# Optimization experiments

Hardware: AMD Instinct MI355X
Metric: run time of the kernel (lower is better)

Reference implementation:

```python
import jax, jax.numpy as jnp
import numpy as np

B, N, DIM, HEADS = 8, 4096, 512, 8
BASE = 10000.0


def rope_cos_sin(n, dim, base=BASE):
    k_max = dim // 2
    theta = 1.0 / base ** (jnp.arange(k_max, dtype=jnp.float32) / k_max)
    angles = jnp.arange(n, dtype=jnp.float32)[:, None] * theta  # (n, k_max)
    return jnp.cos(angles), jnp.sin(angles)


def apply_rope(x, cos, sin):
    # x: (b, n, dim); complex pairs are interleaved (even=real, odd=imag)
    xr = x[..., 0::2]
    xi = x[..., 1::2]
    out_r = cos * xr - sin * xi
    out_i = sin * xr + cos * xi
    return jnp.stack([out_r, out_i], axis=-1).reshape(x.shape)


def setup_inputs() -> dict:
    key = jax.random.key(0)
    ks = jax.random.split(key, 8)
    s = 0.02
    return {
        'x': jax.random.normal(ks[0], (B, N, DIM), jnp.float32),
        'y': jax.random.normal(ks[1], (B, N, DIM), jnp.float32),
        'Wq': jax.random.normal(ks[2], (DIM, DIM), jnp.float32) * s,
        'bq': jax.random.normal(ks[3], (DIM,), jnp.float32) * s,
        'Wk': jax.random.normal(ks[4], (DIM, DIM), jnp.float32) * s,
        'bk': jax.random.normal(ks[5], (DIM,), jnp.float32) * s,
        'lepe_w': jax.random.normal(ks[6], (DIM, 1, 3), jnp.float32) * s,
        'lepe_b': jax.random.normal(ks[7], (DIM,), jnp.float32) * s,
    }


def reference(x, y, Wq, bq, Wk, bk, lepe_w, lepe_b):
    b, n, c = x.shape
    h = HEADS
    d = c // h
    q = jax.nn.elu(x @ Wq.T + bq) + 1.0
    k = jax.nn.elu(y @ Wk.T + bk) + 1.0
    cos, sin = rope_cos_sin(n, c)
    q_rope = apply_rope(q, cos, sin).reshape(b, n, h, d).transpose(0, 2, 1, 3)
    k_rope = apply_rope(k, cos, sin).reshape(b, n, h, d).transpose(0, 2, 1, 3)
    qh = q.reshape(b, n, h, d).transpose(0, 2, 1, 3)
    kh = k.reshape(b, n, h, d).transpose(0, 2, 1, 3)
    v = y.reshape(b, n, h, d).transpose(0, 2, 1, 3)
    kmean = kh.mean(axis=2, keepdims=True)  # (b,h,1,d)
    z = 1.0 / (jnp.einsum('bhnd,bhmd->bhnm', qh, kmean) + 1e-6)  # (b,h,n,1)
    scale = n ** (-0.5)
    kv = jnp.einsum('bhnd,bhne->bhde', k_rope * scale, v * scale)  # (b,h,d,d)
    out = jnp.einsum('bhnd,bhde->bhne', q_rope, kv) * z  # (b,h,n,d)
    out = out.transpose(0, 2, 1, 3).reshape(b, n, c)
    # LePE: depthwise conv1d over value stream
    vc = v.transpose(0, 2, 1, 3).reshape(b, n, c).transpose(0, 2, 1)  # (b,c,n)
    lepe = jax.lax.conv_general_dilated(
        vc, lepe_w, window_strides=(1,), padding=[(1, 1)],
        dimension_numbers=('NCH', 'OIH', 'NCH'), feature_group_count=c)
    lepe = lepe + lepe_b[None, :, None]
    return out + lepe.transpose(0, 2, 1)
```

## Files before the change

kernel.cpp:

```cpp
#include <hip/hip_runtime.h>

#define B_ 8
#define N_ 4096
#define C_ 512
#define H_ 8

typedef _Float16 h8  __attribute__((ext_vector_type(8)));
typedef _Float16 h4v __attribute__((ext_vector_type(4)));
typedef float    f4  __attribute__((ext_vector_type(4)));

static const size_t OFF_CT   = 0;
static const size_t OFF_XH   = (size_t)8*1024*1024;
static const size_t OFF_YH   = (size_t)40*1024*1024;
static const size_t OFF_WQH  = (size_t)72*1024*1024;
static const size_t OFF_WKH  = (size_t)72*1024*1024 + 512*1024;
static const size_t OFF_KSUM = (size_t)73*1024*1024;
static const size_t OFF_KVG  = (size_t)73*1024*1024 + 64*1024;
static const size_t OFF_KVT  = (size_t)74*1024*1024 + 64*1024;

__device__ __forceinline__ unsigned int pack2h(float a, float b){
    union { _Float16 h[2]; unsigned int u; } x;
    x.h[0] = (_Float16)a; x.h[1] = (_Float16)b; return x.u;
}
__device__ __forceinline__ void unpack2h(unsigned int u, float& a, float& b){
    union { unsigned int u; _Float16 h[2]; } x; x.u = u;
    a = (float)x.h[0]; b = (float)x.h[1];
}

__global__ __launch_bounds__(256) void k_prep(
    const float* __restrict__ y,
    const float* __restrict__ Wq, const float* __restrict__ Wk,
    _Float16* __restrict__ yh,
    _Float16* __restrict__ Wqh, _Float16* __restrict__ Wkh,
    unsigned int* __restrict__ ct)
{
    int bid = blockIdx.x;
    if (bid >= 8448){
        int jj = bid - 8448, t = threadIdx.x;
        double th = exp((double)jj * -0.035977892078031970);
        float thf = (float)th;
#pragma unroll
        for (int i=0;i<16;++i){
            int n = i*256 + t;
            float s, c; sincosf((float)n * thf, &s, &c);
            ct[(size_t)jj*4096 + n] = pack2h(c, s);
        }
        return;
    }
    const float* src; _Float16* dst; size_t base;
    if (bid < 8192)       { src = y;  dst = yh;  base = (size_t)bid*2048; }
    else if (bid < 8320)  { src = Wq; dst = Wqh; base = (size_t)(bid-8192)*2048; }
    else                  { src = Wk; dst = Wkh; base = (size_t)(bid-8320)*2048; }
    size_t o = base + (size_t)threadIdx.x*8;
    float4 a = *(const float4*)&src[o];
    float4 b = *(const float4*)&src[o+4];
    uint4 r; r.x = pack2h(a.x,a.y); r.y = pack2h(a.z,a.w); r.z = pack2h(b.x,b.y); r.w = pack2h(b.z,b.w);
    *(uint4*)&dst[o] = r;
}

__device__ __forceinline__ void stage_a64(const _Float16* __restrict__ g, _Float16* lds, int t){
    int r = t >> 2;
    int j = (t & 3) ^ ((r ^ (r >> 2)) & 3);
    __builtin_amdgcn_global_load_lds(
        (const __attribute__((address_space(1))) void*)(g + (size_t)r*C_ + j*8),
        (__attribute__((address_space(3))) void*)(lds + (size_t)(t & 192)*8),
        16, 0, 0);
}
__device__ __forceinline__ void stage_b128(const _Float16* __restrict__ g, _Float16* lds, int t){
#pragma unroll
    for (int i=0;i<2;++i){
        int u = i*256 + t;
        int r = u >> 2;
        int j = (u & 3) ^ ((r ^ (r >> 2)) & 3);
        __builtin_amdgcn_global_load_lds(
            (const __attribute__((address_space(1))) void*)(g + (size_t)r*C_ + j*8),
            (__attribute__((address_space(3))) void*)(lds + (size_t)(i*256 + (t & 192))*8),
            16, 0, 0);
    }
}

template<int IS_Q>
__global__ __launch_bounds__(256, 4) void k_gemm(
    const _Float16* __restrict__ A, const _Float16* __restrict__ Wh, const float* __restrict__ bias,
    const unsigned int* __restrict__ ct,
    float* __restrict__ ksum, const float* __restrict__ ksumIn,
    float* __restrict__ kvg, const _Float16* __restrict__ kvTg,
    const _Float16* __restrict__ yh, const float* __restrict__ lw, const float* __restrict__ lb,
    float* __restrict__ outp,
    const float* __restrict__ x32, _Float16* __restrict__ xh16)
{
    __shared__ __align__(16) char smem[36864];
    _Float16* qrs = (_Float16*)smem;
    unsigned int* krsU = (unsigned int*)smem;
    unsigned int* vsU  = (unsigned int*)(smem + 16384);

    if constexpr (!IS_Q){
        if (blockIdx.y >= 512){
            int cb = (blockIdx.y - 512)*4 + blockIdx.x;
#pragma unroll 4
            for (int it=0; it<32; ++it){
                size_t o = ((size_t)(cb*32 + it))*2048 + (size_t)threadIdx.x*8;
                float4 a = *(const float4*)&x32[o];
                float4 b = *(const float4*)&x32[o+4];
                uint4 r; r.x = pack2h(a.x,a.y); r.y = pack2h(a.z,a.w);
                r.z = pack2h(b.x,b.y); r.w = pack2h(b.z,b.w);
                *(uint4*)&xh16[o] = r;
            }
            return;
        }
    }

    const int t = threadIdx.x;
    const int lane = t & 63;
    const int w = t >> 6;
    const int wm = w >> 1, wn = w & 1;
    const int d_lin = blockIdx.x + (blockIdx.y << 2);
    const int xcd = d_lin & 7;
    const int sq  = d_lin >> 3;
    const int col0 = (sq & 3) * 128;
    const int row0 = (xcd * 64 + (sq >> 2)) * 64;
    const int lrow = lane & 15, lg = lane >> 4;
    const int b = row0 >> 12;

    f4 acc[2][4] = {};
    const _Float16* Ab = A  + (size_t)row0*C_;
    const _Float16* Bb = Wh + (size_t)col0*C_;
    stage_a64 (Ab,      (_Float16*)(smem),               t);
    stage_b128(Bb,      (_Float16*)(smem + 12288),       t);
    stage_a64 (Ab + 32, (_Float16*)(smem + 4096),        t);
    stage_b128(Bb + 32, (_Float16*)(smem + 12288 + 8192),t);

    const int sw = (lrow ^ (lrow >> 2)) & 3;
    const int cK = (lg ^ sw) * 8;

#pragma unroll
    for (int kk=0; kk<16; ++kk){
        if (kk < 15) asm volatile("s_waitcnt vmcnt(3)" ::: "memory");
        else         asm volatile("s_waitcnt vmcnt(0)" ::: "memory");
        __builtin_amdgcn_s_barrier();
        if (kk < 14){
            const int ss = (kk+2)%3;
            stage_a64 (Ab + (kk+2)*32, (_Float16*)(smem + ss*4096),         t);
            stage_b128(Bb + (kk+2)*32, (_Float16*)(smem + 12288 + ss*8192), t);
        }
        const int sc = kk%3;
        const _Float16* As = (const _Float16*)(smem + sc*4096);
        const _Float16* Bs = (const _Float16*)(smem + 12288 + sc*8192);
        h8 af[2], bf[4];
#pragma unroll
        for (int mi=0; mi<2; ++mi) af[mi] = *(const h8*)&As[(wm*32 + mi*16 + lrow)*32 + cK];
#pragma unroll
        for (int ni=0; ni<4; ++ni) bf[ni] = *(const h8*)&Bs[(wn*64 + ni*16 + lrow)*32 + cK];
#pragma unroll
        for (int mi=0; mi<2; ++mi)
#pragma unroll
            for (int ni=0; ni<4; ++ni)
                acc[mi][ni] = __builtin_amdgcn_mfma_f32_16x16x32_f16(af[mi], bf[ni], acc[mi][ni], 0,0,0);
    }
    __syncthreads();

    const int hcol0 = col0 + wn*64;
    float bcol[4], km[4];
#pragma unroll
    for (int ni=0; ni<4; ++ni){
        int c = hcol0 + ni*16 + lrow;
        bcol[ni] = bias[c];
        km[ni] = IS_Q ? ksumIn[b*C_ + c] * (1.0f/4096.0f) : 0.0f;
    }
    float colsum[4] = {0.f,0.f,0.f,0.f};
    float zr[2][4];
    _Float16* qw = qrs + w*2304;

#pragma unroll
    for (int mi=0; mi<2; ++mi){
        float qv[4][4];
#pragma unroll
        for (int ni=0; ni<4; ++ni)
#pragma unroll
            for (int r=0; r<4; ++r){
                float v = acc[mi][ni][r] + bcol[ni];
                qv[ni][r] = v > 0.f ? v + 1.f : __expf(v);
            }
        if constexpr (IS_Q){
#pragma unroll
            for (int r=0; r<4; ++r){
                float p = qv[0][r]*km[0] + qv[1][r]*km[1] + qv[2][r]*km[2] + qv[3][r]*km[3];
                p += __shfl_xor(p, 1); p += __shfl_xor(p, 2);
                p += __shfl_xor(p, 4); p += __shfl_xor(p, 8);
                zr[mi][r] = 1.0f / (p + 1e-6f);
            }
        } else {
#pragma unroll
            for (int ni=0; ni<4; ++ni)
                colsum[ni] += qv[ni][0]+qv[ni][1]+qv[ni][2]+qv[ni][3];
        }
        const int n0 = (row0 & (N_-1)) + wm*32 + mi*16 + lg*4;
#pragma unroll
        for (int ni=0; ni<4; ++ni){
            int c = hcol0 + ni*16 + lrow;
            int jj = c >> 1;
            uint4 tu = *(const uint4*)&ct[(size_t)jj*4096 + n0];
            float cs4[4], sn4[4];
            unpack2h(tu.x, cs4[0], sn4[0]);
            unpack2h(tu.y, cs4[1], sn4[1]);
            unpack2h(tu.z, cs4[2], sn4[2]);
            unpack2h(tu.w, cs4[3], sn4[3]);
            float rv[4];
#pragma unroll
            for (int r=0; r<4; ++r){
                float val = qv[ni][r];
                float par = __shfl_xor(val, 1);
                rv[r] = (lane & 1) ? fmaf(sn4[r], par, cs4[r]*val) : fmaf(cs4[r], val, -sn4[r]*par);
            }
            if constexpr (IS_Q){
#pragma unroll
                for (int r=0; r<4; ++r){
                    float prv = __shfl_xor(rv[r], 1);
                    if (!(lane & 1))
                        *(unsigned int*)&qw[(mi*16 + lg*4 + r)*72 + (ni*16 + lrow)] = pack2h(rv[r], prv);
                }
            } else {
                int d = ni*16 + lrow;
                int n2 = wm*16 + mi*8 + lg*2;
                unsigned int* p = &krsU[wn*2048 + d*32 + (n2 ^ ((d & 7) << 2))];
                uint2 pr; pr.x = pack2h(rv[0], rv[1]); pr.y = pack2h(rv[2], rv[3]);
                *(uint2*)p = pr;
            }
        }
    }

    if constexpr (!IS_Q){
#pragma unroll
        for (int ni=0; ni<4; ++ni){
            float s = colsum[ni];
            s += __shfl_xor(s, 16); s += __shfl_xor(s, 32);
            if (lane < 16) atomicAdd(&ksum[b*C_ + hcol0 + ni*16 + lane], s);
        }
        {
            const int grp = lane >> 4, li = lane & 15;
#pragma unroll
            for (int it=0; it<8; ++it){
                int g = it*4 + w;
                int hl = g >> 4, q = g & 15;
                int row = q*4 + grp;
                uint2 mine = *(const uint2*)&yh[(size_t)(row0 + row)*C_ + col0 + hl*64 + li*4];
                uint2 oth; oth.x = __shfl_xor(mine.x, 16); oth.y = __shfl_xor(mine.y, 16);
                if (!(grp & 1)){
                    int n2 = row >> 1;
#pragma unroll
                    for (int e=0; e<4; ++e){
                        int ea = li*4 + e;
                        unsigned int mf = ((e<2 ? mine.x : mine.y) >> ((e&1)*16)) & 0xffffu;
                        unsigned int of = ((e<2 ? oth.x  : oth.y ) >> ((e&1)*16)) & 0xffffu;
                        vsU[hl*2048 + ea*32 + (n2 ^ ((ea & 7) << 2))] = mf | (of << 16);
                    }
                }
            }
        }
        __syncthreads();
        f4 acc2[2][4] = {};
        const unsigned int* krsW = krsU + wn*2048;
        const unsigned int* vsW  = vsU  + wn*2048;
#pragma unroll
        for (int ks=0; ks<2; ++ks){
            h8 a2[2], b2[4];
#pragma unroll
            for (int mi2=0; mi2<2; ++mi2){
                int d = wm*32 + mi2*16 + lrow;
                int c4 = (ks*16 + lg*4) ^ ((d & 7) << 2);
                a2[mi2] = *(const h8*)&krsW[d*32 + c4];
            }
#pragma unroll
            for (int ni2=0; ni2<4; ++ni2){
                int e = ni2*16 + lrow;
                int c4 = (ks*16 + lg*4) ^ ((e & 7) << 2);
                b2[ni2] = *(const h8*)&vsW[e*32 + c4];
            }
#pragma unroll
            for (int mi2=0; mi2<2; ++mi2)
#pragma unroll
                for (int ni2=0; ni2<4; ++ni2)
                    acc2[mi2][ni2] = __builtin_amdgcn_mfma_f32_16x16x32_f16(a2[mi2], b2[ni2], acc2[mi2][ni2], 0,0,0);
        }
        const int bh = b*H_ + (col0 >> 6) + wn;
#pragma unroll
        for (int mi2=0; mi2<2; ++mi2)
#pragma unroll
            for (int ni2=0; ni2<4; ++ni2)
#pragma unroll
                for (int rr=0; rr<4; ++rr){
                    int d = wm*32 + mi2*16 + lg*4 + rr;
                    int e = ni2*16 + lrow;
                    atomicAdd(&kvg[(size_t)bh*4096 + d*64 + e], acc2[mi2][ni2][rr] * (1.0f/4096.0f));
                }
    } else {
        const int bhh = b*H_ + (col0 >> 6) + wn;
        h8 kv0[4], kv1[4];
#pragma unroll
        for (int ni2=0; ni2<4; ++ni2){
            int e = ni2*16 + lrow;
            kv0[ni2] = *(const h8*)&kvTg[(size_t)bhh*4096 + e*64 + lg*8];
            kv1[ni2] = *(const h8*)&kvTg[(size_t)bhh*4096 + e*64 + 32 + lg*8];
        }
        __syncthreads();
        f4 acc2[2][4] = {};
#pragma unroll
        for (int mi2=0; mi2<2; ++mi2){
            h8 a0 = *(const h8*)&qw[(mi2*16 + lrow)*72 + 0*32 + lg*8];
            h8 a1 = *(const h8*)&qw[(mi2*16 + lrow)*72 + 1*32 + lg*8];
#pragma unroll
            for (int ni2=0; ni2<4; ++ni2){
                acc2[mi2][ni2] = __builtin_amdgcn_mfma_f32_16x16x32_f16(a0, kv0[ni2], acc2[mi2][ni2], 0,0,0);
                acc2[mi2][ni2] = __builtin_amdgcn_mfma_f32_16x16x32_f16(a1, kv1[ni2], acc2[mi2][ni2], 0,0,0);
            }
        }
#pragma unroll
        for (int mi2=0; mi2<2; ++mi2){
#pragma unroll
            for (int r=0; r<4; ++r){
                float z = zr[mi2][r];
#pragma unroll
                for (int ni2=0; ni2<4; ++ni2){
                    float val = acc2[mi2][ni2][r] * z;
                    float pv = __shfl_xor(val, 1);
                    if (!(lane & 1))
                        *(unsigned int*)&qw[(mi2*16 + lg*4 + r)*72 + (ni2*16 + lrow)] = pack2h(val, pv);
                }
            }
        }
        __syncthreads();
        const int cg = t & 31;
        const int c4p = cg * 4;
        const int hl = c4p >> 6;
        const int e0 = c4p & 63;
        float w0[4], w1[4], w2[4], wb[4];
#pragma unroll
        for (int j=0;j<4;++j){
            int cc = col0 + c4p + j;
            w0[j]=lw[cc*3+0]; w1[j]=lw[cc*3+1]; w2[j]=lw[cc*3+2]; wb[j]=lb[cc];
        }
#pragma unroll
        for (int i=0;i<8;++i){
            int rl = (t >> 5) + i*8;
            int grow = row0 + rl;
            int nloc = grow & (N_-1);
            int wreg = ((rl >> 5) << 1) + hl;
            h4v a = *(const h4v*)&qrs[wreg*2304 + (rl & 31)*72 + e0];
            const _Float16* yp = yh + (size_t)grow*C_ + col0 + c4p;
            h4v y1 = *(const h4v*)yp;
            float s0 = fmaf((float)y1[0], w1[0], wb[0]);
            float s1 = fmaf((float)y1[1], w1[1], wb[1]);
            float s2 = fmaf((float)y1[2], w1[2], wb[2]);
            float s3 = fmaf((float)y1[3], w1[3], wb[3]);
            if (nloc > 0){
                h4v y0 = *(const h4v*)(yp - C_);
                s0 = fmaf((float)y0[0], w0[0], s0); s1 = fmaf((float)y0[1], w0[1], s1);
                s2 = fmaf((float)y0[2], w0[2], s2); s3 = fmaf((float)y0[3], w0[3], s3);
            }
            if (nloc < N_-1){
                h4v y2 = *(const h4v*)(yp + C_);
                s0 = fmaf((float)y2[0], w2[0], s0); s1 = fmaf((float)y2[1], w2[1], s1);
                s2 = fmaf((float)y2[2], w2[2], s2); s3 = fmaf((float)y2[3], w2[3], s3);
            }
            float4 o;
            o.x = (float)a[0] + s0; o.y = (float)a[1] + s1;
            o.z = (float)a[2] + s2; o.w = (float)a[3] + s3;
            *(float4*)&outp[(size_t)grow*C_ + col0 + c4p] = o;
        }
    }
}

__global__ __launch_bounds__(256) void k_kvmerge(const float* __restrict__ kvg, _Float16* __restrict__ kvTg){
    int bh = blockIdx.x, t = threadIdx.x;
    const float* src = kvg + (size_t)bh*4096;
    _Float16* dst = kvTg + (size_t)bh*4096;
#pragma unroll
    for (int i=0;i<4;++i){
        int q = i*256 + t;
        int e2 = q & 31, d2 = q >> 5;
        float2 a0 = *(const float2*)&src[(2*d2)*64 + 2*e2];
        float2 a1 = *(const float2*)&src[(2*d2+1)*64 + 2*e2];
        *(unsigned int*)&dst[(2*e2)*64 + 2*d2]   = pack2h(a0.x, a1.x);
        *(unsigned int*)&dst[(2*e2+1)*64 + 2*d2] = pack2h(a0.y, a1.y);
    }
}

extern "C" void kernel_launch(void* const* d_in, const int* in_sizes, int n_in,
                              void* d_out, int out_size, void* d_ws, size_t ws_size,
                              hipStream_t stream)
{
    (void)in_sizes; (void)n_in; (void)out_size; (void)ws_size;
    const float* x  = (const float*)d_in[0];
    const float* y  = (const float*)d_in[1];
    const float* Wq = (const float*)d_in[2];
    const float* bq = (const float*)d_in[3];
    const float* Wk = (const float*)d_in[4];
    const float* bk = (const float*)d_in[5];
    const float* lw = (const float*)d_in[6];
    const float* lb = (const float*)d_in[7];

    char* ws = (char*)d_ws;
    unsigned int* ct = (unsigned int*)(ws + OFF_CT);
    _Float16* xh   = (_Float16*)(ws + OFF_XH);
    _Float16* yh   = (_Float16*)(ws + OFF_YH);
    _Float16* Wqh  = (_Float16*)(ws + OFF_WQH);
    _Float16* Wkh  = (_Float16*)(ws + OFF_WKH);
    float*    ksum = (float*)(ws + OFF_KSUM);
    float*    kvg  = (float*)(ws + OFF_KVG);
    _Float16* kvTg = (_Float16*)(ws + OFF_KVT);
    float*    out  = (float*)d_out;

    hipMemsetAsync(ws + OFF_KSUM, 0, 64*1024 + 1024*1024, stream);
    k_prep<<<dim3(8704), dim3(256), 0, stream>>>(y, Wq, Wk, yh, Wqh, Wkh, ct);
    k_gemm<0><<<dim3(4, 576), dim3(256), 0, stream>>>(yh, Wkh, bk, ct,
        ksum, nullptr, kvg, nullptr, yh, nullptr, nullptr, nullptr, x, xh);
    k_kvmerge<<<dim3(64), dim3(256), 0, stream>>>(kvg, kvTg);
    k_gemm<1><<<dim3(4, 512), dim3(256), 0, stream>>>(xh, Wqh, bq, ct,
        nullptr, ksum, nullptr, kvTg, yh, lw, lb, out, nullptr, nullptr);
}
```

Measured before the change: 185.2 us.

## Switch projection GEMMs to single-wave blocks reading operands directly from global

Both GEMM kernels now launch one 64-thread wavefront per block, with 64x64 tiles for K and 32x64 tiles for Q. Each block covers exactly one head's columns. The LDS-staged triple-buffered global_load_lds pipeline and its barriers are removed, so MFMA fragments load straight from global memory into registers. The aim is to cut barrier and LDS traffic and raise occupancy through more, smaller blocks. The cost is redundant global and L2 reads of the A and W operands with no shared-memory reuse across waves.

```diff
diff --git a/kernel.cpp b/kernel.cpp
--- a/kernel.cpp
+++ b/kernel.cpp
@@ -58,29 +58,8 @@
     *(uint4*)&dst[o] = r;
 }
 
-__device__ __forceinline__ void stage_a64(const _Float16* __restrict__ g, _Float16* lds, int t){
-    int r = t >> 2;
-    int j = (t & 3) ^ ((r ^ (r >> 2)) & 3);
-    __builtin_amdgcn_global_load_lds(
-        (const __attribute__((address_space(1))) void*)(g + (size_t)r*C_ + j*8),
-        (__attribute__((address_space(3))) void*)(lds + (size_t)(t & 192)*8),
-        16, 0, 0);
-}
-__device__ __forceinline__ void stage_b128(const _Float16* __restrict__ g, _Float16* lds, int t){
-#pragma unroll
-    for (int i=0;i<2;++i){
-        int u = i*256 + t;
-        int r = u >> 2;
-        int j = (u & 3) ^ ((r ^ (r >> 2)) & 3);
-        __builtin_amdgcn_global_load_lds(
-            (const __attribute__((address_space(1))) void*)(g + (size_t)r*C_ + j*8),
-            (__attribute__((address_space(3))) void*)(lds + (size_t)(i*256 + (t & 192))*8),
-            16, 0, 0);
-    }
-}
-
-template<int IS_Q>
-__global__ __launch_bounds__(256, 4) void k_gemm(
+template<int IS_Q, int MI>
+__global__ __launch_bounds__(64, IS_Q ? 4 : 3) void k_gemm(
     const _Float16* __restrict__ A, const _Float16* __restrict__ Wh, const float* __restrict__ bias,
     const unsigned int* __restrict__ ct,
     float* __restrict__ ksum, const float* __restrict__ ksumIn,
@@ -89,17 +68,18 @@
     float* __restrict__ outp,
     const float* __restrict__ x32, _Float16* __restrict__ xh16)
 {
-    __shared__ __align__(16) char smem[36864];
-    _Float16* qrs = (_Float16*)smem;
-    unsigned int* krsU = (unsigned int*)smem;
-    unsigned int* vsU  = (unsigned int*)(smem + 16384);
+    __shared__ __align__(16) char smem[IS_Q ? 4608 : 16384];
+    _Float16* qw = (_Float16*)smem;
+    unsigned int* krU = (unsigned int*)smem;
+    unsigned int* vU  = (unsigned int*)(smem + 8192);
 
     if constexpr (!IS_Q){
         if (blockIdx.y >= 512){
-            int cb = (blockIdx.y - 512)*4 + blockIdx.x;
+            int cb = (blockIdx.y - 512)*8 + blockIdx.x;
+            int t = threadIdx.x;
 #pragma unroll 4
-            for (int it=0; it<32; ++it){
-                size_t o = ((size_t)(cb*32 + it))*2048 + (size_t)threadIdx.x*8;
+            for (int it=0; it<128; ++it){
+                size_t o = ((size_t)cb*128 + it)*512 + (size_t)t*8;
                 float4 a = *(const float4*)&x32[o];
                 float4 b = *(const float4*)&x32[o+4];
                 uint4 r; r.x = pack2h(a.x,a.y); r.y = pack2h(a.z,a.w);
@@ -111,68 +91,43 @@
     }
 
     const int t = threadIdx.x;
-    const int lane = t & 63;
-    const int w = t >> 6;
-    const int wm = w >> 1, wn = w & 1;
-    const int d_lin = blockIdx.x + (blockIdx.y << 2);
-    const int xcd = d_lin & 7;
-    const int sq  = d_lin >> 3;
-    const int col0 = (sq & 3) * 128;
-    const int row0 = (xcd * 64 + (sq >> 2)) * 64;
-    const int lrow = lane & 15, lg = lane >> 4;
+    const int lrow = t & 15, lg = t >> 4;
+    const int d_lin = blockIdx.x + (blockIdx.y << 3);
+    const int xcd = d_lin & 7, s = d_lin >> 3;
+    const int col0 = (s & 7) * 64;
+    const int row0 = IS_Q ? (xcd*128 + (s >> 3))*32 : (xcd*64 + (s >> 3))*64;
     const int b = row0 >> 12;
-
-    f4 acc[2][4] = {};
-    const _Float16* Ab = A  + (size_t)row0*C_;
-    const _Float16* Bb = Wh + (size_t)col0*C_;
-    stage_a64 (Ab,      (_Float16*)(smem),               t);
-    stage_b128(Bb,      (_Float16*)(smem + 12288),       t);
-    stage_a64 (Ab + 32, (_Float16*)(smem + 4096),        t);
-    stage_b128(Bb + 32, (_Float16*)(smem + 12288 + 8192),t);
-
-    const int sw = (lrow ^ (lrow >> 2)) & 3;
-    const int cK = (lg ^ sw) * 8;
-
+    const int bh = b*H_ + (col0 >> 6);
+
+    f4 acc[MI][4] = {};
+    const _Float16* pa = A  + ((size_t)(row0 + lrow))*C_ + lg*8;
+    const _Float16* pb = Wh + ((size_t)(col0 + lrow))*C_ + lg*8;
 #pragma unroll
     for (int kk=0; kk<16; ++kk){
-        if (kk < 15) asm volatile("s_waitcnt vmcnt(3)" ::: "memory");
-        else         asm volatile("s_waitcnt vmcnt(0)" ::: "memory");
-        __builtin_amdgcn_s_barrier();
-        if (kk < 14){
-            const int ss = (kk+2)%3;
-            stage_a64 (Ab + (kk+2)*32, (_Float16*)(smem + ss*4096),         t);
-            stage_b128(Bb + (kk+2)*32, (_Float16*)(smem + 12288 + ss*8192), t);
-        }
-        const int sc = kk%3;
-        const _Float16* As = (const _Float16*)(smem + sc*4096);
-        const _Float16* Bs = (const _Float16*)(smem + 12288 + sc*8192);
-        h8 af[2], bf[4];
-#pragma unroll
-        for (int mi=0; mi<2; ++mi) af[mi] = *(const h8*)&As[(wm*32 + mi*16 + lrow)*32 + cK];
-#pragma unroll
-        for (int ni=0; ni<4; ++ni) bf[ni] = *(const h8*)&Bs[(wn*64 + ni*16 + lrow)*32 + cK];
-#pragma unroll
-        for (int mi=0; mi<2; ++mi)
+        h8 af[MI], bf[4];
+#pragma unroll
+        for (int mi=0; mi<MI; ++mi) af[mi] = *(const h8*)(pa + (size_t)mi*16*C_ + kk*32);
+#pragma unroll
+        for (int ni=0; ni<4; ++ni)  bf[ni] = *(const h8*)(pb + (size_t)ni*16*C_ + kk*32);
+#pragma unroll
+        for (int mi=0; mi<MI; ++mi)
 #pragma unroll
             for (int ni=0; ni<4; ++ni)
                 acc[mi][ni] = __builtin_amdgcn_mfma_f32_16x16x32_f16(af[mi], bf[ni], acc[mi][ni], 0,0,0);
     }
-    __syncthreads();
-
-    const int hcol0 = col0 + wn*64;
+
     float bcol[4], km[4];
 #pragma unroll
     for (int ni=0; ni<4; ++ni){
-        int c = hcol0 + ni*16 + lrow;
+        int c = col0 + ni*16 + lrow;
         bcol[ni] = bias[c];
         km[ni] = IS_Q ? ksumIn[b*C_ + c] * (1.0f/4096.0f) : 0.0f;
     }
     float colsum[4] = {0.f,0.f,0.f,0.f};
-    float zr[2][4];
-    _Float16* qw = qrs + w*2304;
-
-#pragma unroll
-    for (int mi=0; mi<2; ++mi){
+    float zr[MI][4];
+
+#pragma unroll
+    for (int mi=0; mi<MI; ++mi){
         float qv[4][4];
 #pragma unroll
         for (int ni=0; ni<4; ++ni)
@@ -194,10 +149,10 @@
             for (int ni=0; ni<4; ++ni)
                 colsum[ni] += qv[ni][0]+qv[ni][1]+qv[ni][2]+qv[ni][3];
         }
-        const int n0 = (row0 & (N_-1)) + wm*32 + mi*16 + lg*4;
+        const int n0 = (row0 & (N_-1)) + mi*16 + lg*4;
 #pragma unroll
         for (int ni=0; ni<4; ++ni){
-            int c = hcol0 + ni*16 + lrow;
+            int c = col0 + ni*16 + lrow;
             int jj = c >> 1;
             uint4 tu = *(const uint4*)&ct[(size_t)jj*4096 + n0];
             float cs4[4], sn4[4];
@@ -210,19 +165,19 @@
             for (int r=0; r<4; ++r){
                 float val = qv[ni][r];
                 float par = __shfl_xor(val, 1);
-                rv[r] = (lane & 1) ? fmaf(sn4[r], par, cs4[r]*val) : fmaf(cs4[r], val, -sn4[r]*par);
+                rv[r] = (t & 1) ? fmaf(sn4[r], par, cs4[r]*val) : fmaf(cs4[r], val, -sn4[r]*par);
             }
             if constexpr (IS_Q){
 #pragma unroll
                 for (int r=0; r<4; ++r){
                     float prv = __shfl_xor(rv[r], 1);
-                    if (!(lane & 1))
+                    if (!(t & 1))
                         *(unsigned int*)&qw[(mi*16 + lg*4 + r)*72 + (ni*16 + lrow)] = pack2h(rv[r], prv);
                 }
             } else {
-                int d = ni*16 + lrow;
-                int n2 = wm*16 + mi*8 + lg*2;
-                unsigned int* p = &krsU[wn*2048 + d*32 + (n2 ^ ((d & 7) << 2))];
+                int dd = ni*16 + lrow;
+                int n2 = mi*8 + lg*2;
+                unsigned int* p = &krU[dd*32 + (n2 ^ ((dd & 7) << 2))];
                 uint2 pr; pr.x = pack2h(rv[0], rv[1]); pr.y = pack2h(rv[2], rv[3]);
                 *(uint2*)p = pr;
             }
@@ -232,75 +187,65 @@
     if constexpr (!IS_Q){
 #pragma unroll
         for (int ni=0; ni<4; ++ni){
-            float s = colsum[ni];
-            s += __shfl_xor(s, 16); s += __shfl_xor(s, 32);
-            if (lane < 16) atomicAdd(&ksum[b*C_ + hcol0 + ni*16 + lane], s);
-        }
-        {
-            const int grp = lane >> 4, li = lane & 15;
-#pragma unroll
-            for (int it=0; it<8; ++it){
-                int g = it*4 + w;
-                int hl = g >> 4, q = g & 15;
-                int row = q*4 + grp;
-                uint2 mine = *(const uint2*)&yh[(size_t)(row0 + row)*C_ + col0 + hl*64 + li*4];
-                uint2 oth; oth.x = __shfl_xor(mine.x, 16); oth.y = __shfl_xor(mine.y, 16);
-                if (!(grp & 1)){
-                    int n2 = row >> 1;
-#pragma unroll
-                    for (int e=0; e<4; ++e){
-                        int ea = li*4 + e;
-                        unsigned int mf = ((e<2 ? mine.x : mine.y) >> ((e&1)*16)) & 0xffffu;
-                        unsigned int of = ((e<2 ? oth.x  : oth.y ) >> ((e&1)*16)) & 0xffffu;
-                        vsU[hl*2048 + ea*32 + (n2 ^ ((ea & 7) << 2))] = mf | (of << 16);
-                    }
-                }
-            }
+            float ss = colsum[ni];
+            ss += __shfl_xor(ss, 16); ss += __shfl_xor(ss, 32);
+            if (t < 16) atomicAdd(&ksum[b*C_ + col0 + ni*16 + t], ss);
+        }
+#pragma unroll
+        for (int it=0; it<8; ++it){
+            int n2g = it*4 + lg;
+            int e4 = lrow*4;
+            uint2 r0 = *(const uint2*)&yh[(size_t)(row0 + 2*n2g)*C_ + col0 + e4];
+            uint2 r1 = *(const uint2*)&yh[(size_t)(row0 + 2*n2g + 1)*C_ + col0 + e4];
+            unsigned int v0 = (r0.x & 0xffffu) | (r1.x << 16);
+            unsigned int v1 = (r0.x >> 16)     | (r1.x & 0xffff0000u);
+            unsigned int v2 = (r0.y & 0xffffu) | (r1.y << 16);
+            unsigned int v3 = (r0.y >> 16)     | (r1.y & 0xffff0000u);
+            vU[(e4+0)*32 + (n2g ^ (((e4+0) & 7) << 2))] = v0;
+            vU[(e4+1)*32 + (n2g ^ (((e4+1) & 7) << 2))] = v1;
+            vU[(e4+2)*32 + (n2g ^ (((e4+2) & 7) << 2))] = v2;
+            vU[(e4+3)*32 + (n2g ^ (((e4+3) & 7) << 2))] = v3;
         }
         __syncthreads();
-        f4 acc2[2][4] = {};
-        const unsigned int* krsW = krsU + wn*2048;
-        const unsigned int* vsW  = vsU  + wn*2048;
+        f4 acc2[4][4] = {};
 #pragma unroll
         for (int ks=0; ks<2; ++ks){
-            h8 a2[2], b2[4];
-#pragma unroll
-            for (int mi2=0; mi2<2; ++mi2){
-                int d = wm*32 + mi2*16 + lrow;
-                int c4 = (ks*16 + lg*4) ^ ((d & 7) << 2);
-                a2[mi2] = *(const h8*)&krsW[d*32 + c4];
+            h8 a2[4], b2[4];
+#pragma unroll
+            for (int mi2=0; mi2<4; ++mi2){
+                int dd = mi2*16 + lrow;
+                int c4 = (ks*16 + lg*4) ^ ((dd & 7) << 2);
+                a2[mi2] = *(const h8*)&krU[dd*32 + c4];
             }
 #pragma unroll
             for (int ni2=0; ni2<4; ++ni2){
                 int e = ni2*16 + lrow;
                 int c4 = (ks*16 + lg*4) ^ ((e & 7) << 2);
-                b2[ni2] = *(const h8*)&vsW[e*32 + c4];
-            }
-#pragma unroll
-            for (int mi2=0; mi2<2; ++mi2)
+                b2[ni2] = *(const h8*)&vU[e*32 + c4];
+            }
+#pragma unroll
+            for (int mi2=0; mi2<4; ++mi2)
 #pragma unroll
                 for (int ni2=0; ni2<4; ++ni2)
                     acc2[mi2][ni2] = __builtin_amdgcn_mfma_f32_16x16x32_f16(a2[mi2], b2[ni2], acc2[mi2][ni2], 0,0,0);
         }
-        const int bh = b*H_ + (col0 >> 6) + wn;
-#pragma unroll
-        for (int mi2=0; mi2<2; ++mi2)
+#pragma unroll
+        for (int mi2=0; mi2<4; ++mi2)
 #pragma unroll
             for (int ni2=0; ni2<4; ++ni2)
 #pragma unroll
                 for (int rr=0; rr<4; ++rr){
-                    int d = wm*32 + mi2*16 + lg*4 + rr;
+                    int dd = mi2*16 + lg*4 + rr;
                     int e = ni2*16 + lrow;
-                    atomicAdd(&kvg[(size_t)bh*4096 + d*64 + e], acc2[mi2][ni2][rr] * (1.0f/4096.0f));
+                    atomicAdd(&kvg[(size_t)bh*4096 + dd*64 + e], acc2[mi2][ni2][rr] * (1.0f/4096.0f));
                 }
     } else {
-        const int bhh = b*H_ + (col0 >> 6) + wn;
         h8 kv0[4], kv1[4];
 #pragma unroll
         for (int ni2=0; ni2<4; ++ni2){
             int e = ni2*16 + lrow;
-            kv0[ni2] = *(const h8*)&kvTg[(size_t)bhh*4096 + e*64 + lg*8];
-            kv1[ni2] = *(const h8*)&kvTg[(size_t)bhh*4096 + e*64 + 32 + lg*8];
+            kv0[ni2] = *(const h8*)&kvTg[(size_t)bh*4096 + e*64 + lg*8];
+            kv1[ni2] = *(const h8*)&kvTg[(size_t)bh*4096 + e*64 + 32 + lg*8];
         }
         __syncthreads();
         f4 acc2[2][4] = {};
@@ -323,30 +268,26 @@
                 for (int ni2=0; ni2<4; ++ni2){
                     float val = acc2[mi2][ni2][r] * z;
                     float pv = __shfl_xor(val, 1);
-                    if (!(lane & 1))
+                    if (!(t & 1))
                         *(unsigned int*)&qw[(mi2*16 + lg*4 + r)*72 + (ni2*16 + lrow)] = pack2h(val, pv);
                 }
             }
         }
         __syncthreads();
-        const int cg = t & 31;
-        const int c4p = cg * 4;
-        const int hl = c4p >> 6;
-        const int e0 = c4p & 63;
+        const int e4 = (t & 15)*4;
         float w0[4], w1[4], w2[4], wb[4];
 #pragma unroll
         for (int j=0;j<4;++j){
-            int cc = col0 + c4p + j;
+            int cc = col0 + e4 + j;
             w0[j]=lw[cc*3+0]; w1[j]=lw[cc*3+1]; w2[j]=lw[cc*3+2]; wb[j]=lb[cc];
         }
 #pragma unroll
         for (int i=0;i<8;++i){
-            int rl = (t >> 5) + i*8;
+            int rl = i*4 + lg;
             int grow = row0 + rl;
             int nloc = grow & (N_-1);
-            int wreg = ((rl >> 5) << 1) + hl;
-            h4v a = *(const h4v*)&qrs[wreg*2304 + (rl & 31)*72 + e0];
-            const _Float16* yp = yh + (size_t)grow*C_ + col0 + c4p;
+            h4v a = *(const h4v*)&qw[rl*72 + e4];
+            const _Float16* yp = yh + (size_t)grow*C_ + col0 + e4;
             h4v y1 = *(const h4v*)yp;
             float s0 = fmaf((float)y1[0], w1[0], wb[0]);
             float s1 = fmaf((float)y1[1], w1[1], wb[1]);
@@ -365,7 +306,7 @@
             float4 o;
             o.x = (float)a[0] + s0; o.y = (float)a[1] + s1;
             o.z = (float)a[2] + s2; o.w = (float)a[3] + s3;
-            *(float4*)&outp[(size_t)grow*C_ + col0 + c4p] = o;
+            *(float4*)&outp[(size_t)grow*C_ + col0 + e4] = o;
         }
     }
 }
@@ -412,9 +353,9 @@
 
     hipMemsetAsync(ws + OFF_KSUM, 0, 64*1024 + 1024*1024, stream);
     k_prep<<<dim3(8704), dim3(256), 0, stream>>>(y, Wq, Wk, yh, Wqh, Wkh, ct);
-    k_gemm<0><<<dim3(4, 576), dim3(256), 0, stream>>>(yh, Wkh, bk, ct,
+    k_gemm<0,4><<<dim3(8, 544), dim3(64), 0, stream>>>(yh, Wkh, bk, ct,
         ksum, nullptr, kvg, nullptr, yh, nullptr, nullptr, nullptr, x, xh);
     k_kvmerge<<<dim3(64), dim3(256), 0, stream>>>(kvg, kvTg);
-    k_gemm<1><<<dim3(4, 512), dim3(256), 0, stream>>>(xh, Wqh, bq, ct,
+    k_gemm<1,2><<<dim3(8, 1024), dim3(64), 0, stream>>>(xh, Wqh, bq, ct,
         nullptr, ksum, nullptr, kvTg, yh, lw, lb, out, nullptr, nullptr);
 }
```

New measurement: 281.4 us. +52.0%, slower.
